# Kernel optimization log

Measured on AMD Instinct MI355X. Metric: run time of the kernel, lower is better.

## Reference

```python
import jax, jax.numpy as jnp
import numpy as np

NUM_HEADS = 16
HEAD_DIM = 64
ROPE_BASE = 10000.0


def _rope_cos_sin(seq_len, head_dim, dtype):
    inv_freq = 1.0 / (ROPE_BASE ** (jnp.arange(0, head_dim, 2, dtype=jnp.float32) / head_dim))
    t = jnp.arange(seq_len, dtype=jnp.float32)
    freqs = t[:, None] * inv_freq[None, :]          # (S, head_dim/2)
    emb = jnp.concatenate([freqs, freqs], axis=-1)  # (S, head_dim)
    return jnp.cos(emb).astype(dtype), jnp.sin(emb).astype(dtype)


def _rotate_half(x):
    x1, x2 = jnp.split(x, 2, axis=-1)
    return jnp.concatenate([-x2, x1], axis=-1)


def setup_inputs() -> dict:
    key = jax.random.key(0)
    k1, k2, k3 = jax.random.split(key, 3)
    B, S, D = 2, 2048, 1024
    x = jax.random.normal(k1, (B, S, D), dtype=jnp.float32)
    Wq = jax.random.normal(k2, (D, D), dtype=jnp.float32) * (D ** -0.5)
    Wkv = jax.random.normal(k3, (2 * D, D), dtype=jnp.float32) * (D ** -0.5)
    mask = jnp.tril(jnp.ones((S, S), dtype=jnp.int32))  # causal mask
    return {"x": x, "Wq": Wq, "Wkv": Wkv, "mask": mask}


def reference(x, Wq, Wkv, mask):
    B, S, D = x.shape
    H, Hd = NUM_HEADS, HEAD_DIM

    # projections (torch Linear: x @ W.T)
    q = (x @ Wq.T).reshape(B, S, H, Hd).transpose(0, 2, 1, 3)           # (B,H,S,Hd)
    kv = (x @ Wkv.T).reshape(B, S, H, Hd, 2).transpose(0, 2, 1, 3, 4)   # (B,H,S,Hd,2)
    k = kv[..., 0]
    v = kv[..., 1]

    # RoPE
    cos, sin = _rope_cos_sin(S, Hd, x.dtype)  # (S,Hd) broadcast over (B,H)
    q = q * cos + _rotate_half(q) * sin
    k = k * cos + _rotate_half(k) * sin

    # attention with full score materialization (faithful to source)
    scale = 1.0 / jnp.sqrt(jnp.asarray(Hd, dtype=x.dtype))
    scores = jnp.einsum('bhqd,bhkd->bhqk', q, k) * scale                # (B,H,S,S)
    scores = jnp.where(mask == 0, -jnp.inf, scores)
    attn = jax.nn.softmax(scores, axis=-1)
    out = jnp.einsum('bhqk,bhkd->bhqd', attn, v)                        # (B,H,S,Hd)
    return out.transpose(0, 2, 1, 3).reshape(B, S, D)
```

## Files before the change

kernel.cpp:

```cpp
#include <hip/hip_runtime.h>
#include <hip/hip_bf16.h>
#include <math.h>


typedef short bfrag __attribute__((ext_vector_type(8)));
typedef float f32x4 __attribute__((ext_vector_type(4)));

__device__ __forceinline__ float bf2f(ushort u) {
    union { uint i; float f; } v; v.i = ((uint)u) << 16; return v.f;
}
__device__ __forceinline__ ushort f2bf(float f) {
    union { uint i; float f; } v; v.f = f;
    uint u = v.i;
    return (ushort)((u + 0x7fffu + ((u >> 16) & 1u)) >> 16);
}

#define MFMA16 __builtin_amdgcn_mfma_f32_16x16x32_bf16

__device__ __forceinline__ void gl_lds16(const ushort* g, ushort* l) {
    __builtin_amdgcn_global_load_lds(
        (const __attribute__((address_space(1))) void*)g,
        (__attribute__((address_space(3))) void*)l, 16, 0, 0);
}

__global__ __launch_bounds__(256)
void cvt_bf16(const float* __restrict__ x, const float* __restrict__ wq,
              const float* __restrict__ wkv, ushort* __restrict__ xb,
              ushort* __restrict__ wb)
{
    const size_t NX = 4096u * 1024u, NWQ = 1024u * 1024u;
    size_t i8 = ((size_t)blockIdx.x * 256 + threadIdx.x) * 8;
    const float* src;
    ushort* dst;
    if (i8 < NX) { src = x + i8; dst = xb + i8; }
    else {
        size_t j = i8 - NX;
        dst = wb + j;
        src = (j < NWQ) ? (wq + j) : (wkv + (j - NWQ));
    }
    float4 a = *(const float4*)(src);
    float4 c = *(const float4*)(src + 4);
    ushort u[8];
    u[0] = f2bf(a.x); u[1] = f2bf(a.y); u[2] = f2bf(a.z); u[3] = f2bf(a.w);
    u[4] = f2bf(c.x); u[5] = f2bf(c.y); u[6] = f2bf(c.z); u[7] = f2bf(c.w);
    *(uint4*)dst = *(uint4*)u;
}

__global__ __launch_bounds__(256)
void rope_table(float2* __restrict__ tab)
{
    int t  = blockIdx.x * 256 + threadIdx.x;
    int fi = t & 31, s = t >> 5;
    float invf = (float)exp((double)fi * -0.28782313662425574);
    float thf  = (float)s * invf;
    const double TWO_PI = 6.283185307179586476925287;
    double th = (double)thf;
    double kq = __builtin_rint(th * (1.0 / TWO_PI));
    float r = (float)(th - kq * TWO_PI);
    tab[t] = make_float2(cosf(r), sinf(r));
}

__global__ __launch_bounds__(256)
void gemm_qkv(const ushort* __restrict__ xb, const ushort* __restrict__ wb,
              const float2* __restrict__ tab, ushort* __restrict__ Qb,
              ushort* __restrict__ Kb, ushort* __restrict__ Vt)
{
    __shared__ ushort Ash[128][32];
    __shared__ ushort Bsh[128][32];

    const int tid  = threadIdx.x;
    const int lane = tid & 63, wv = tid >> 6;
    const int quad = lane >> 4, li = lane & 15;
    const int m0 = blockIdx.x * 128, n0 = blockIdx.y * 128;

    f32x4 acc[2][8];
#pragma unroll
    for (int mi = 0; mi < 2; mi++)
#pragma unroll
        for (int j = 0; j < 8; j++) acc[mi][j] = (f32x4){0.f, 0.f, 0.f, 0.f};

    const int rsub = lane >> 2, kofs = (lane & 3) * 8;
    const ushort* gA0 = xb + (size_t)(m0 + wv * 32 + rsub) * 1024 + kofs;
    const ushort* gA1 = gA0 + 16 * 1024;
    const ushort* gB0 = wb + (size_t)(n0 + wv * 32 + rsub) * 1024 + kofs;
    const ushort* gB1 = gB0 + 16 * 1024;

    for (int k0 = 0; k0 < 1024; k0 += 32) {
        __syncthreads();
        gl_lds16(gA0 + k0, &Ash[wv * 32][0]);
        gl_lds16(gA1 + k0, &Ash[wv * 32 + 16][0]);
        gl_lds16(gB0 + k0, &Bsh[wv * 32][0]);
        gl_lds16(gB1 + k0, &Bsh[wv * 32 + 16][0]);
        __syncthreads();

        bfrag af[2], bf[8];
#pragma unroll
        for (int mi = 0; mi < 2; mi++)
            af[mi] = *(const bfrag*)&Ash[wv * 32 + mi * 16 + li][quad * 8];
#pragma unroll
        for (int j = 0; j < 8; j++)
            bf[j] = *(const bfrag*)&Bsh[j * 16 + li][quad * 8];
#pragma unroll
        for (int mi = 0; mi < 2; mi++)
#pragma unroll
            for (int j = 0; j < 8; j++)
                acc[mi][j] = MFMA16(af[mi], bf[j], acc[mi][j], 0, 0, 0);
    }

    if (n0 < 1024) {
        const int hbase = n0 >> 6;
#pragma unroll
        for (int mi = 0; mi < 2; mi++)
#pragma unroll
            for (int r = 0; r < 4; r++) {
                int m = m0 + wv * 32 + mi * 16 + quad * 4 + r;
                int bb = m >> 11, s = m & 2047;
                float2 t0 = tab[s * 32 + li];
                float2 t1 = tab[s * 32 + li + 16];
#pragma unroll
                for (int j = 0; j < 8; j++) {
                    float v  = acc[mi][j][r];
                    float vp = acc[mi][j ^ 2][r];
                    float2 tt = (j & 1) ? t1 : t0;
                    float rh = (j & 2) ? vp : -vp;
                    int h = hbase + (j >> 2), hd = (j & 3) * 16 + li;
                    Qb[(size_t)((bb * 16 + h) * 2048 + s) * 64 + hd] =
                        f2bf(v * tt.x + rh * tt.y);
                }
            }
    } else {
        const int h = (n0 - 1024) >> 7;
        const int li2 = li >> 1;
        if ((li & 1) == 0) {
#pragma unroll
            for (int mi = 0; mi < 2; mi++)
#pragma unroll
                for (int r = 0; r < 4; r++) {
                    int m = m0 + wv * 32 + mi * 16 + quad * 4 + r;
                    int bb = m >> 11, s = m & 2047;
                    float2 tt4[4];
#pragma unroll
                    for (int jj = 0; jj < 4; jj++)
                        tt4[jj] = tab[s * 32 + jj * 8 + li2];
#pragma unroll
                    for (int j = 0; j < 8; j++) {
                        float v  = acc[mi][j][r];
                        float vp = acc[mi][j ^ 4][r];
                        float2 tt = tt4[j & 3];
                        float rh = (j & 4) ? vp : -vp;
                        int hd = j * 8 + li2;
                        Kb[(size_t)((bb * 16 + h) * 2048 + s) * 64 + hd] =
                            f2bf(v * tt.x + rh * tt.y);
                    }
                }
        } else {
#pragma unroll
            for (int mi = 0; mi < 2; mi++) {
                int m4 = m0 + wv * 32 + mi * 16 + quad * 4;
                int bb = m4 >> 11, s0 = m4 & 2047;
#pragma unroll
                for (int j = 0; j < 8; j++) {
                    int hd = j * 8 + li2;
                    ushort u4[4];
#pragma unroll
                    for (int r = 0; r < 4; r++) u4[r] = f2bf(acc[mi][j][r]);
                    *(ushort4*)&Vt[(size_t)((bb * 16 + h) * 64 + hd) * 2048 + s0] =
                        *(ushort4*)u4;
                }
            }
        }
    }
}

__global__ __launch_bounds__(256)
void attn(const ushort* __restrict__ Qb, const ushort* __restrict__ Kb,
          const ushort* __restrict__ Vt, float* __restrict__ out)
{
    __shared__ ushort Ksh[64][72];
    __shared__ ushort Vsh[64][72];
    __shared__ ushort Psh[4][16][72];

    const int tid  = threadIdx.x;
    const int lane = tid & 63, w = tid >> 6;
    const int quad = lane >> 4, li = lane & 15;
    const int qt = ((31 - (int)blockIdx.x) + (int)blockIdx.y) & 31;
    const int bh = blockIdx.y;
    const int b = bh >> 4, h = bh & 15;

    const int qrow = qt * 64 + w * 16 + li;
    const ushort* qp = Qb + (size_t)(bh * 2048 + qrow) * 64;
    bfrag qa0 = *(const bfrag*)(qp + quad * 8);
    bfrag qa1 = *(const bfrag*)(qp + quad * 8 + 32);

    f32x4 o[4];
#pragma unroll
    for (int j = 0; j < 4; j++) o[j] = (f32x4){0.f, 0.f, 0.f, 0.f};
    float lrow = 0.f;

    const int srow = tid >> 2, sc0 = (tid & 3) * 16;
    const ushort* kbase = Kb + (size_t)bh * 2048 * 64;
    const ushort* vbase = Vt + (size_t)bh * 64 * 2048;

    uint4 ka, kb_, va, vb_;
    {
        const ushort* gk = kbase + (size_t)srow * 64 + sc0;
        ka  = *(const uint4*)gk;
        kb_ = *(const uint4*)(gk + 8);
        const ushort* gv = vbase + (size_t)srow * 2048 + sc0;
        va  = *(const uint4*)gv;
        vb_ = *(const uint4*)(gv + 8);
    }

    const float C = 0.125f * 1.4426950408889634f;

    for (int kt = 0; kt <= qt; ++kt) {
        __syncthreads();
        *(uint4*)&Ksh[srow][sc0]     = ka;
        *(uint4*)&Ksh[srow][sc0 + 8] = kb_;
        *(uint4*)&Vsh[srow][sc0]     = va;
        *(uint4*)&Vsh[srow][sc0 + 8] = vb_;
        __syncthreads();

        if (kt < qt) {
            const ushort* gk = kbase + (size_t)((kt + 1) * 64 + srow) * 64 + sc0;
            ka  = *(const uint4*)gk;
            kb_ = *(const uint4*)(gk + 8);
            const ushort* gv = vbase + (size_t)srow * 2048 + (kt + 1) * 64 + sc0;
            va  = *(const uint4*)gv;
            vb_ = *(const uint4*)(gv + 8);
        }

        f32x4 sc[4];
        __builtin_amdgcn_s_setprio(1);
#pragma unroll
        for (int j = 0; j < 4; j++) {
            bfrag kb0 = *(const bfrag*)&Ksh[j * 16 + li][quad * 8];
            bfrag kb1 = *(const bfrag*)&Ksh[j * 16 + li][quad * 8 + 32];
            f32x4 z = (f32x4){0.f, 0.f, 0.f, 0.f};
            z = MFMA16(kb0, qa0, z, 0, 0, 0);
            z = MFMA16(kb1, qa1, z, 0, 0, 0);
            sc[j] = z;
        }
        __builtin_amdgcn_s_setprio(0);

        if (kt == qt) {
#pragma unroll
            for (int j = 0; j < 4; j++) {
                int kg0 = kt * 64 + j * 16 + quad * 4;
#pragma unroll
                for (int r = 0; r < 4; r++)
                    sc[j][r] = (kg0 + r <= qrow) ? sc[j][r] : -3.0e38f;
            }
        }

        float rs = 0.f;
#pragma unroll
        for (int j = 0; j < 4; j++) {
            ushort pk[4];
#pragma unroll
            for (int r = 0; r < 4; r++) {
                float pv = exp2f(sc[j][r] * C);
                uint pu = __float_as_uint(pv);
                pk[r] = (ushort)(pu >> 16);
                rs += __uint_as_float(pu & 0xffff0000u);
            }
            *(ushort4*)&Psh[w][li][j * 16 + quad * 4] = *(ushort4*)pk;
        }
        rs += __shfl_xor(rs, 16);
        rs += __shfl_xor(rs, 32);
        lrow += rs;

        asm volatile("s_waitcnt lgkmcnt(0)" ::: "memory");
        bfrag pa0 = *(const bfrag*)&Psh[w][li][quad * 8];
        bfrag pa1 = *(const bfrag*)&Psh[w][li][quad * 8 + 32];

        __builtin_amdgcn_s_setprio(1);
#pragma unroll
        for (int j = 0; j < 4; j++) {
            bfrag vb0 = *(const bfrag*)&Vsh[j * 16 + li][quad * 8];
            bfrag vb1 = *(const bfrag*)&Vsh[j * 16 + li][quad * 8 + 32];
            o[j] = MFMA16(pa0, vb0, o[j], 0, 0, 0);
            o[j] = MFMA16(pa1, vb1, o[j], 0, 0, 0);
        }
        __builtin_amdgcn_s_setprio(0);
    }

    float lf[4];
#pragma unroll
    for (int r = 0; r < 4; r++)
        lf[r] = __shfl(lrow, (lane & 48) + quad * 4 + r);

#pragma unroll
    for (int j = 0; j < 4; j++)
#pragma unroll
        for (int r = 0; r < 4; r++) {
            int s = qt * 64 + w * 16 + quad * 4 + r;
            out[(size_t)(b * 2048 + s) * 1024 + h * 64 + j * 16 + li] =
                o[j][r] / lf[r];
        }
}

extern "C" void kernel_launch(void* const* d_in, const int* in_sizes, int n_in,
                              void* d_out, int out_size, void* d_ws, size_t ws_size,
                              hipStream_t stream)
{
    (void)in_sizes; (void)n_in; (void)out_size; (void)ws_size;
    const float* x   = (const float*)d_in[0];
    const float* wq  = (const float*)d_in[1];
    const float* wkv = (const float*)d_in[2];

    ushort* xb = (ushort*)d_ws;
    ushort* wb = xb + (size_t)4096 * 1024;
    float2* tab = (float2*)(wb + (size_t)3072 * 1024);
    ushort* Qb = (ushort*)(tab + 65536);
    ushort* Kb = Qb + (size_t)2 * 16 * 2048 * 64;
    ushort* Vt = Kb + (size_t)2 * 16 * 2048 * 64;
    float* out = (float*)d_out;

    cvt_bf16<<<3584, 256, 0, stream>>>(x, wq, wkv, xb, wb);
    rope_table<<<256, 256, 0, stream>>>(tab);
    dim3 g1(32, 24);
    gemm_qkv<<<g1, 256, 0, stream>>>(xb, wb, tab, Qb, Kb, Vt);
    dim3 g4(32, 32);
    attn<<<g4, 256, 0, stream>>>(Qb, Kb, Vt, out);
}
```

Measured before the change: 189.0 us.

## Pair short and long causal query tiles per block to share K/V loads

Each attention block now processes two query tiles, t and 31-t, so every block does the same amount of causal work and the staged K/V tiles are reused for both. The grid is halved from 32x32 to 16x32 blocks. This is meant to remove load imbalance from the causal triangle and to cut redundant K/V global loads and LDS staging. In exchange it raises register pressure from the doubled accumulators and Q fragments, and adds branches on doS inside the inner loop.

```diff
diff --git a/kernel.cpp b/kernel.cpp
--- a/kernel.cpp
+++ b/kernel.cpp
@@ -178,24 +178,35 @@
 {
     __shared__ ushort Ksh[64][72];
     __shared__ ushort Vsh[64][72];
-    __shared__ ushort Psh[4][16][72];
+    __shared__ ushort Psh[8][16][80];
 
     const int tid  = threadIdx.x;
     const int lane = tid & 63, w = tid >> 6;
     const int quad = lane >> 4, li = lane & 15;
-    const int qt = ((31 - (int)blockIdx.x) + (int)blockIdx.y) & 31;
-    const int bh = blockIdx.y;
+
+    const int l  = (int)blockIdx.y * 16 + (int)blockIdx.x;
+    const int bh = l & 31;
+    const int i  = l >> 5;
+    const int t  = (i < 8) ? i : 23 - i;
+    const int qtS = t, qtB = 31 - t;
     const int b = bh >> 4, h = bh & 15;
 
-    const int qrow = qt * 64 + w * 16 + li;
-    const ushort* qp = Qb + (size_t)(bh * 2048 + qrow) * 64;
-    bfrag qa0 = *(const bfrag*)(qp + quad * 8);
-    bfrag qa1 = *(const bfrag*)(qp + quad * 8 + 32);
-
-    f32x4 o[4];
-#pragma unroll
-    for (int j = 0; j < 4; j++) o[j] = (f32x4){0.f, 0.f, 0.f, 0.f};
-    float lrow = 0.f;
+    const int rowB = qtB * 64 + w * 16 + li;
+    const int rowS = qtS * 64 + w * 16 + li;
+    const ushort* qpB = Qb + (size_t)(bh * 2048 + rowB) * 64;
+    const ushort* qpS = Qb + (size_t)(bh * 2048 + rowS) * 64;
+    bfrag qaB0 = *(const bfrag*)(qpB + quad * 8);
+    bfrag qaB1 = *(const bfrag*)(qpB + quad * 8 + 32);
+    bfrag qaS0 = *(const bfrag*)(qpS + quad * 8);
+    bfrag qaS1 = *(const bfrag*)(qpS + quad * 8 + 32);
+
+    f32x4 oB[4], oS[4];
+#pragma unroll
+    for (int j = 0; j < 4; j++) {
+        oB[j] = (f32x4){0.f, 0.f, 0.f, 0.f};
+        oS[j] = (f32x4){0.f, 0.f, 0.f, 0.f};
+    }
+    float lrowB = 0.f, lrowS = 0.f;
 
     const int srow = tid >> 2, sc0 = (tid & 3) * 16;
     const ushort* kbase = Kb + (size_t)bh * 2048 * 64;
@@ -213,7 +224,7 @@
 
     const float C = 0.125f * 1.4426950408889634f;
 
-    for (int kt = 0; kt <= qt; ++kt) {
+    for (int kt = 0; kt <= qtB; ++kt) {
         __syncthreads();
         *(uint4*)&Ksh[srow][sc0]     = ka;
         *(uint4*)&Ksh[srow][sc0 + 8] = kb_;
@@ -221,7 +232,7 @@
         *(uint4*)&Vsh[srow][sc0 + 8] = vb_;
         __syncthreads();
 
-        if (kt < qt) {
+        if (kt < qtB) {
             const ushort* gk = kbase + (size_t)((kt + 1) * 64 + srow) * 64 + sc0;
             ka  = *(const uint4*)gk;
             kb_ = *(const uint4*)(gk + 8);
@@ -230,73 +241,111 @@
             vb_ = *(const uint4*)(gv + 8);
         }
 
-        f32x4 sc[4];
-        __builtin_amdgcn_s_setprio(1);
+        const bool doS = (kt <= qtS);
+        float rsB = 0.f, rsS = 0.f;
+
 #pragma unroll
         for (int j = 0; j < 4; j++) {
-            bfrag kb0 = *(const bfrag*)&Ksh[j * 16 + li][quad * 8];
-            bfrag kb1 = *(const bfrag*)&Ksh[j * 16 + li][quad * 8 + 32];
-            f32x4 z = (f32x4){0.f, 0.f, 0.f, 0.f};
-            z = MFMA16(kb0, qa0, z, 0, 0, 0);
-            z = MFMA16(kb1, qa1, z, 0, 0, 0);
-            sc[j] = z;
-        }
-        __builtin_amdgcn_s_setprio(0);
-
-        if (kt == qt) {
-#pragma unroll
-            for (int j = 0; j < 4; j++) {
+            bfrag kf0 = *(const bfrag*)&Ksh[j * 16 + li][quad * 8];
+            bfrag kf1 = *(const bfrag*)&Ksh[j * 16 + li][quad * 8 + 32];
+
+            __builtin_amdgcn_s_setprio(1);
+            f32x4 zB = (f32x4){0.f, 0.f, 0.f, 0.f};
+            zB = MFMA16(kf0, qaB0, zB, 0, 0, 0);
+            zB = MFMA16(kf1, qaB1, zB, 0, 0, 0);
+            f32x4 zS = (f32x4){0.f, 0.f, 0.f, 0.f};
+            if (doS) {
+                zS = MFMA16(kf0, qaS0, zS, 0, 0, 0);
+                zS = MFMA16(kf1, qaS1, zS, 0, 0, 0);
+            }
+            __builtin_amdgcn_s_setprio(0);
+
+            if (kt == qtB) {
                 int kg0 = kt * 64 + j * 16 + quad * 4;
 #pragma unroll
                 for (int r = 0; r < 4; r++)
-                    sc[j][r] = (kg0 + r <= qrow) ? sc[j][r] : -3.0e38f;
-            }
-        }
-
-        float rs = 0.f;
+                    zB[r] = (kg0 + r <= rowB) ? zB[r] : -3.0e38f;
+            }
+            if (doS && kt == qtS) {
+                int kg0 = kt * 64 + j * 16 + quad * 4;
+#pragma unroll
+                for (int r = 0; r < 4; r++)
+                    zS[r] = (kg0 + r <= rowS) ? zS[r] : -3.0e38f;
+            }
+
+            ushort pkB[4];
+#pragma unroll
+            for (int r = 0; r < 4; r++) {
+                float pv = exp2f(zB[r] * C);
+                uint pu = __float_as_uint(pv);
+                pkB[r] = (ushort)(pu >> 16);
+                rsB += __uint_as_float(pu & 0xffff0000u);
+            }
+            *(ushort4*)&Psh[w * 2][li][j * 16 + quad * 4] = *(ushort4*)pkB;
+
+            if (doS) {
+                ushort pkS[4];
+#pragma unroll
+                for (int r = 0; r < 4; r++) {
+                    float pv = exp2f(zS[r] * C);
+                    uint pu = __float_as_uint(pv);
+                    pkS[r] = (ushort)(pu >> 16);
+                    rsS += __uint_as_float(pu & 0xffff0000u);
+                }
+                *(ushort4*)&Psh[w * 2 + 1][li][j * 16 + quad * 4] = *(ushort4*)pkS;
+            }
+        }
+
+        rsB += __shfl_xor(rsB, 16);
+        rsB += __shfl_xor(rsB, 32);
+        lrowB += rsB;
+        if (doS) {
+            rsS += __shfl_xor(rsS, 16);
+            rsS += __shfl_xor(rsS, 32);
+            lrowS += rsS;
+        }
+
+        asm volatile("s_waitcnt lgkmcnt(0)" ::: "memory");
+        bfrag paB0 = *(const bfrag*)&Psh[w * 2][li][quad * 8];
+        bfrag paB1 = *(const bfrag*)&Psh[w * 2][li][quad * 8 + 32];
+        bfrag paS0, paS1;
+        if (doS) {
+            paS0 = *(const bfrag*)&Psh[w * 2 + 1][li][quad * 8];
+            paS1 = *(const bfrag*)&Psh[w * 2 + 1][li][quad * 8 + 32];
+        }
+
 #pragma unroll
         for (int j = 0; j < 4; j++) {
-            ushort pk[4];
-#pragma unroll
-            for (int r = 0; r < 4; r++) {
-                float pv = exp2f(sc[j][r] * C);
-                uint pu = __float_as_uint(pv);
-                pk[r] = (ushort)(pu >> 16);
-                rs += __uint_as_float(pu & 0xffff0000u);
-            }
-            *(ushort4*)&Psh[w][li][j * 16 + quad * 4] = *(ushort4*)pk;
-        }
-        rs += __shfl_xor(rs, 16);
-        rs += __shfl_xor(rs, 32);
-        lrow += rs;
-
-        asm volatile("s_waitcnt lgkmcnt(0)" ::: "memory");
-        bfrag pa0 = *(const bfrag*)&Psh[w][li][quad * 8];
-        bfrag pa1 = *(const bfrag*)&Psh[w][li][quad * 8 + 32];
-
-        __builtin_amdgcn_s_setprio(1);
-#pragma unroll
-        for (int j = 0; j < 4; j++) {
-            bfrag vb0 = *(const bfrag*)&Vsh[j * 16 + li][quad * 8];
-            bfrag vb1 = *(const bfrag*)&Vsh[j * 16 + li][quad * 8 + 32];
-            o[j] = MFMA16(pa0, vb0, o[j], 0, 0, 0);
-            o[j] = MFMA16(pa1, vb1, o[j], 0, 0, 0);
-        }
-        __builtin_amdgcn_s_setprio(0);
-    }
-
-    float lf[4];
-#pragma unroll
-    for (int r = 0; r < 4; r++)
-        lf[r] = __shfl(lrow, (lane & 48) + quad * 4 + r);
+            bfrag vf0 = *(const bfrag*)&Vsh[j * 16 + li][quad * 8];
+            bfrag vf1 = *(const bfrag*)&Vsh[j * 16 + li][quad * 8 + 32];
+            __builtin_amdgcn_s_setprio(1);
+            oB[j] = MFMA16(paB0, vf0, oB[j], 0, 0, 0);
+            oB[j] = MFMA16(paB1, vf1, oB[j], 0, 0, 0);
+            if (doS) {
+                oS[j] = MFMA16(paS0, vf0, oS[j], 0, 0, 0);
+                oS[j] = MFMA16(paS1, vf1, oS[j], 0, 0, 0);
+            }
+            __builtin_amdgcn_s_setprio(0);
+        }
+    }
+
+    float lfB[4], lfS[4];
+#pragma unroll
+    for (int r = 0; r < 4; r++) {
+        lfB[r] = __shfl(lrowB, (lane & 48) + quad * 4 + r);
+        lfS[r] = __shfl(lrowS, (lane & 48) + quad * 4 + r);
+    }
 
 #pragma unroll
     for (int j = 0; j < 4; j++)
 #pragma unroll
         for (int r = 0; r < 4; r++) {
-            int s = qt * 64 + w * 16 + quad * 4 + r;
-            out[(size_t)(b * 2048 + s) * 1024 + h * 64 + j * 16 + li] =
-                o[j][r] / lf[r];
+            int sB = qtB * 64 + w * 16 + quad * 4 + r;
+            out[(size_t)(b * 2048 + sB) * 1024 + h * 64 + j * 16 + li] =
+                oB[j][r] / lfB[r];
+            int sS = qtS * 64 + w * 16 + quad * 4 + r;
+            out[(size_t)(b * 2048 + sS) * 1024 + h * 64 + j * 16 + li] =
+                oS[j][r] / lfS[r];
         }
 }
 
@@ -321,6 +370,6 @@
     rope_table<<<256, 256, 0, stream>>>(tab);
     dim3 g1(32, 24);
     gemm_qkv<<<g1, 256, 0, stream>>>(xb, wb, tab, Qb, Kb, Vt);
-    dim3 g4(32, 32);
+    dim3 g4(16, 32);
     attn<<<g4, 256, 0, stream>>>(Qb, Kb, Vt, out);
 }
```

Measured after the change: 186.6 us. Within noise of the previous version (-1.3%).
